# Optimization experiments

Hardware: AMD Instinct MI355X
Metric: run time of the kernel (lower is better)

Reference implementation:

```python
import jax, jax.numpy as jnp
import numpy as np

DIM = 1024
N_HEADS = 16
HEAD_DIM = DIM // N_HEADS
BATCH = 2
SEQ = 2048


def rotate_half(x):
    x1, x2 = jnp.split(x, 2, axis=-1)
    return jnp.concatenate((-x2, x1), axis=-1)


def rope_cos_sin(seq_len, head_dim, dtype=jnp.float32):
    inv_freq = 1.0 / (10000.0 ** (jnp.arange(0, head_dim, 2, dtype=jnp.float32) / head_dim))
    t = jnp.arange(seq_len, dtype=jnp.float32)
    freqs = jnp.einsum('i,j->ij', t, inv_freq)          # [S, hd/2]
    emb = jnp.concatenate((freqs, freqs), axis=-1)       # [S, hd]
    return emb.astype(dtype)[None, :, None, :]           # [1, S, 1, hd] (cos/sin applied below)


def setup_inputs() -> dict:
    key = jax.random.key(0)
    k_x, k_q, k_k, k_v, k_o = jax.random.split(key, 5)
    scale = 1.0 / np.sqrt(DIM)
    x = jax.random.normal(k_x, (BATCH, SEQ, DIM), dtype=jnp.float32)
    Wq = jax.random.normal(k_q, (DIM, DIM), dtype=jnp.float32) * scale
    Wk = jax.random.normal(k_k, (DIM, DIM), dtype=jnp.float32) * scale
    Wv = jax.random.normal(k_v, (DIM, DIM), dtype=jnp.float32) * scale
    Wo = jax.random.normal(k_o, (DIM, DIM), dtype=jnp.float32) * scale
    # causal mask: scores masked where mask == 0
    mask = jnp.tril(jnp.ones((SEQ, SEQ), dtype=jnp.int32))[None, None, :, :]
    return {"x": x, "Wq": Wq, "Wk": Wk, "Wv": Wv, "Wo": Wo, "mask": mask}


def reference(x, Wq, Wk, Wv, Wo, mask):
    B, S, _ = x.shape
    # torch nn.Linear: y = x @ W.T
    q = (x @ Wq.T).reshape(B, S, N_HEADS, HEAD_DIM)
    k = (x @ Wk.T).reshape(B, S, N_HEADS, HEAD_DIM)
    v = (x @ Wv.T).reshape(B, S, N_HEADS, HEAD_DIM)
    ang = rope_cos_sin(S, HEAD_DIM, x.dtype)
    cos, sin = jnp.cos(ang), jnp.sin(ang)
    q = q * cos + rotate_half(q) * sin
    k = k * cos + rotate_half(k) * sin
    # [B, H, S, hd]
    q = q.transpose(0, 2, 1, 3)
    k = k.transpose(0, 2, 1, 3)
    v = v.transpose(0, 2, 1, 3)
    scores = jnp.einsum('bhqd,bhkd->bhqk', q, k) / np.sqrt(HEAD_DIM)
    scores = jnp.where(mask == 0, jnp.asarray(-1e9, scores.dtype), scores)
    attn = jax.nn.softmax(scores, axis=-1)
    out = jnp.einsum('bhqk,bhkd->bhqd', attn, v)
    out = out.transpose(0, 2, 1, 3).reshape(B, S, DIM)
    return out @ Wo.T
```

## Files before the change

### kernel.cpp

```cpp
#include <hip/hip_runtime.h>
#include <stdint.h>

typedef unsigned short u16;
typedef __bf16 bf16x8 __attribute__((ext_vector_type(8)));
typedef __bf16 bf16x4 __attribute__((ext_vector_type(4)));
typedef float f32x4 __attribute__((ext_vector_type(4)));

#define N_B 2
#define N_S 2048
#define N_D 1024
#define N_H 16
#define HD 64

#if __has_builtin(__builtin_amdgcn_exp2f)
#define EXP2F(x) __builtin_amdgcn_exp2f(x)
#else
#define EXP2F(x) exp2f(x)
#endif

__device__ __forceinline__ u16 f2bf(float f) {
  union { float f; uint32_t u; } v; v.f = f;
  uint32_t u = v.u + 0x7fffu + ((v.u >> 16) & 1u);
  return (u16)(u >> 16);
}

__device__ __forceinline__ void gload16(const u16* g, u16* lds) {
  __builtin_amdgcn_global_load_lds(
      (const __attribute__((address_space(1))) unsigned int*)g,
      (__attribute__((address_space(3))) unsigned int*)lds, 16, 0, 0);
}

__global__ __launch_bounds__(256) void prep_kernel(
    const float* __restrict__ x, const float* __restrict__ Wq,
    const float* __restrict__ Wk, const float* __restrict__ Wv,
    const float* __restrict__ Wo,
    u16* __restrict__ xb, u16* __restrict__ wqb, u16* __restrict__ wkb,
    u16* __restrict__ wvb, u16* __restrict__ wob,
    float* __restrict__ cosT, float* __restrict__ sinT)
{
  const int NX = N_B * N_S * N_D;
  const int NW = N_D * N_D;
  int bid = blockIdx.x;
  if (bid < 8192) {
    int i = (bid * 256 + threadIdx.x) * 4;
    const float* src; u16* dst; int off;
    if (i < NX) { src = x; dst = xb; off = i; }
    else {
      int j = i - NX;
      int w = j >> 20;
      off = j & (NW - 1);
      src = (w == 0) ? Wq : (w == 1) ? Wk : (w == 2) ? Wv : Wo;
      dst = (w == 0) ? wqb : (w == 1) ? wkb : (w == 2) ? wvb : wob;
    }
    float4 v = *(const float4*)(src + off);
    ushort4 o;
    o.x = f2bf(v.x); o.y = f2bf(v.y); o.z = f2bf(v.z); o.w = f2bf(v.w);
    *(ushort4*)(dst + off) = o;
  } else {
    int t = (bid - 8192) * 256 + threadIdx.x;
    int s = t >> 5, i = t & 31;
    float inv = expf(-(float)i * 0.28782313662425574f);
    float a = (float)s * inv;
    float sn, cs;
    sincosf(a, &sn, &cs);
    cosT[t] = cs;
    sinT[t] = sn;
  }
}

__global__ __launch_bounds__(256, 5) void proj_kernel(
    const u16* __restrict__ x, const u16* __restrict__ Wq,
    const u16* __restrict__ Wk, const u16* __restrict__ Wv,
    u16* __restrict__ Qb, u16* __restrict__ Kb, u16* __restrict__ Vtb,
    const float* __restrict__ cosT, const float* __restrict__ sinT)
{
  const int mode = blockIdx.z;
  const u16* Wm = (mode == 0) ? Wq : (mode == 1) ? Wk : Wv;
  const int bx = blockIdx.x, by = blockIdx.y;
  const int tid = threadIdx.x;
  const int wave = tid >> 6, lane = tid & 63;
  const int c = lane & 15, quad = lane >> 4;

  __shared__ __align__(16) u16 As[128 * 64];
  __shared__ __align__(16) u16 Bs[64 * 64];

  const f32x4 zero = {0.f, 0.f, 0.f, 0.f};
  f32x4 acc[2][4];
#pragma unroll
  for (int i = 0; i < 2; ++i)
#pragma unroll
    for (int j = 0; j < 4; ++j) acc[i][j] = zero;

  for (int kt = 0; kt < 16; ++kt) {
    const int k0 = kt * 64;
    __syncthreads();
#pragma unroll
    for (int t = 0; t < 4; ++t) {
      int p = t * 256 + tid;
      int m = p >> 3, sl = p & 7;
      int kq = sl ^ (m & 7);
      gload16(x + (size_t)(by * 128 + m) * N_D + k0 + kq * 8, &As[(t * 256 + wave * 64) * 8]);
    }
#pragma unroll
    for (int t = 0; t < 2; ++t) {
      int p = t * 256 + tid;
      int m = p >> 3, sl = p & 7;
      int kq = sl ^ (m & 7);
      gload16(Wm + (size_t)(bx * 64 + m) * N_D + k0 + kq * 8, &Bs[(t * 256 + wave * 64) * 8]);
    }
    __syncthreads();
#pragma unroll
    for (int ks = 0; ks < 2; ++ks) {
      bf16x8 av[2], bv[4];
      int kq = ks * 4 + quad;
#pragma unroll
      for (int i = 0; i < 2; ++i) {
        int m = wave * 32 + i * 16 + c;
        av[i] = *(const bf16x8*)&As[(m * 8 + (kq ^ (m & 7))) * 8];
      }
#pragma unroll
      for (int j = 0; j < 4; ++j) {
        int n = j * 16 + c;
        bv[j] = *(const bf16x8*)&Bs[(n * 8 + (kq ^ (n & 7))) * 8];
      }
#pragma unroll
      for (int i = 0; i < 2; ++i)
#pragma unroll
        for (int j = 0; j < 4; ++j)
          acc[i][j] = __builtin_amdgcn_mfma_f32_16x16x32_bf16(av[i], bv[j], acc[i][j], 0, 0, 0);
    }
  }

  const int h = bx;
  if (mode < 2) {
    u16* Out = (mode == 0) ? Qb : Kb;
#pragma unroll
    for (int i = 0; i < 2; ++i) {
#pragma unroll
      for (int r = 0; r < 4; ++r) {
        int row = by * 128 + wave * 32 + i * 16 + quad * 4 + r;
        int b = row >> 11, s = row & 2047;
        float cs0 = cosT[s * 32 + c],      sn0 = sinT[s * 32 + c];
        float cs1 = cosT[s * 32 + 16 + c], sn1 = sinT[s * 32 + 16 + c];
        size_t base = ((size_t)(b * N_H + h) * N_S + s) * HD;
#pragma unroll
        for (int j = 0; j < 4; ++j) {
          float v = acc[i][j][r];
          float p = acc[i][j ^ 2][r];
          float cs = (j & 1) ? cs1 : cs0;
          float sn = (j & 1) ? sn1 : sn0;
          float res = (j < 2) ? (v * cs - p * sn) : (v * cs + p * sn);
          Out[base + j * 16 + c] = f2bf(res);
        }
      }
    }
  } else {
#pragma unroll
    for (int i = 0; i < 2; ++i) {
      int srow = by * 128 + wave * 32 + i * 16 + quad * 4;
      int b = srow >> 11, sb = srow & 2047;
#pragma unroll
      for (int j = 0; j < 4; ++j) {
        int d = j * 16 + c;
        ushort4 pk;
        pk.x = f2bf(acc[i][j][0]);
        pk.y = f2bf(acc[i][j][1]);
        pk.z = f2bf(acc[i][j][2]);
        pk.w = f2bf(acc[i][j][3]);
        *(ushort4*)&Vtb[((size_t)(b * N_H + h) * HD + d) * N_S + sb] = pk;
      }
    }
  }
}

__global__ __launch_bounds__(64, 3) void attn_kernel(
    const u16* __restrict__ Qb, const u16* __restrict__ Kb,
    const u16* __restrict__ Vtb, u16* __restrict__ Ab)
{
  const int lane = threadIdx.x;
  const int c = lane & 15, quad = lane >> 4;
  const int bx = blockIdx.x;
  const int xcd = bx & 7;
  const int idx = bx >> 3;
  const int t = 63 - (idx >> 2);
  const int bh = xcd + (idx & 3) * 8;
  const int q0 = t * 32;
  const int ktmax = t;

  __shared__ __align__(16) u16 Ks[32 * 64];
  __shared__ __align__(16) u16 Vs[64 * 32];
  __shared__ __align__(16) u16 Ps[32 * 32];

  const u16* Qg = Qb + ((size_t)bh * N_S + q0) * HD;
  const u16* Kg = Kb + (size_t)bh * N_S * HD;
  const u16* Vg = Vtb + (size_t)bh * HD * N_S;

  bf16x8 qreg[2][2];
#pragma unroll
  for (int jQ = 0; jQ < 2; ++jQ)
#pragma unroll
    for (int ks = 0; ks < 2; ++ks)
      qreg[jQ][ks] = *(const bf16x8*)(Qg + (jQ * 16 + c) * HD + ks * 32 + quad * 8);

  const f32x4 zero = {0.f, 0.f, 0.f, 0.f};
  f32x4 acc_o[2][4];
#pragma unroll
  for (int mt = 0; mt < 2; ++mt)
#pragma unroll
    for (int nt = 0; nt < 4; ++nt) acc_o[mt][nt] = zero;
  float lrow[2] = {0.f, 0.f};

  const float CLOG = 0.18033688011112042f;
  const float FM = 16.0f;

  for (int kt = 0; kt <= ktmax; ++kt) {
    asm volatile("s_waitcnt lgkmcnt(0)" ::: "memory");
#pragma unroll
    for (int i = 0; i < 4; ++i) {
      int ci = i * 64 + lane;
      int m = ci >> 3, sl = ci & 7;
      int kq = sl ^ (m & 7);
      gload16(Kg + (size_t)(kt * 32 + m) * HD + kq * 8, &Ks[i * 512]);
    }
#pragma unroll
    for (int i = 0; i < 4; ++i) {
      int ci = i * 64 + lane;
      int d = ci >> 2, sl = ci & 3;
      int kq = sl ^ (d & 3);
      gload16(Vg + (size_t)d * N_S + kt * 32 + kq * 8, &Vs[i * 512]);
    }
    asm volatile("s_waitcnt vmcnt(4)" ::: "memory");

    f32x4 acc_s[2][2];
#pragma unroll
    for (int iK = 0; iK < 2; ++iK)
#pragma unroll
      for (int jQ = 0; jQ < 2; ++jQ) acc_s[iK][jQ] = zero;
#pragma unroll
    for (int ks = 0; ks < 2; ++ks) {
      bf16x8 kf[2];
      int kq = ks * 4 + quad;
#pragma unroll
      for (int iK = 0; iK < 2; ++iK) {
        int m = iK * 16 + c;
        kf[iK] = *(const bf16x8*)&Ks[(m * 8 + (kq ^ (m & 7))) * 8];
      }
#pragma unroll
      for (int iK = 0; iK < 2; ++iK)
#pragma unroll
        for (int jQ = 0; jQ < 2; ++jQ)
          acc_s[iK][jQ] = __builtin_amdgcn_mfma_f32_16x16x32_bf16(
              kf[iK], qreg[jQ][ks], acc_s[iK][jQ], 0, 0, 0);
    }

    const bool domask = (kt == ktmax);
#pragma unroll
    for (int iK = 0; iK < 2; ++iK)
#pragma unroll
      for (int jQ = 0; jQ < 2; ++jQ) {
        bf16x4 pb;
#pragma unroll
        for (int rr = 0; rr < 4; ++rr) {
          float arg = fmaf(acc_s[iK][jQ][rr], CLOG, -FM);
          if (domask) {
            int dsk = iK * 16 + quad * 4 + rr;
            int dq = jQ * 16 + c;
            if (dsk > dq) arg = -3.0e38f;
          }
          float p = EXP2F(arg);
          lrow[jQ] += p;
          pb[rr] = (__bf16)p;
        }
        int q = jQ * 16 + c;
        int slot = (iK * 2 + (quad >> 1)) ^ (q & 3);
        *(bf16x4*)&Ps[q * 32 + slot * 8 + (quad & 1) * 4] = pb;
      }

    asm volatile("s_waitcnt vmcnt(0)" ::: "memory");

    bf16x8 pf[2], vf[4];
#pragma unroll
    for (int nt = 0; nt < 4; ++nt) {
      int d = nt * 16 + c;
      vf[nt] = *(const bf16x8*)&Vs[(d * 4 + (quad ^ (d & 3))) * 8];
    }
#pragma unroll
    for (int mt = 0; mt < 2; ++mt) {
      int q = mt * 16 + c;
      pf[mt] = *(const bf16x8*)&Ps[q * 32 + ((quad ^ (q & 3)) * 8)];
    }
#pragma unroll
    for (int mt = 0; mt < 2; ++mt)
#pragma unroll
      for (int nt = 0; nt < 4; ++nt)
        acc_o[mt][nt] = __builtin_amdgcn_mfma_f32_16x16x32_bf16(
            pf[mt], vf[nt], acc_o[mt][nt], 0, 0, 0);
  }

#pragma unroll
  for (int jQ = 0; jQ < 2; ++jQ) {
    float l = lrow[jQ];
    l += __shfl_xor(l, 16, 64);
    l += __shfl_xor(l, 32, 64);
    lrow[jQ] = 1.0f / l;
  }
  const int b = bh >> 4, h = bh & 15;
#pragma unroll
  for (int mt = 0; mt < 2; ++mt) {
#pragma unroll
    for (int rr = 0; rr < 4; ++rr) {
      float inv = __shfl(lrow[mt], quad * 4 + rr, 64);
      int q = q0 + mt * 16 + quad * 4 + rr;
#pragma unroll
      for (int nt = 0; nt < 4; ++nt) {
        Ab[((size_t)(b * N_S + q)) * N_D + h * HD + nt * 16 + c] =
            f2bf(acc_o[mt][nt][rr] * inv);
      }
    }
  }
}

__global__ __launch_bounds__(256) void out_gemm_kernel(
    const u16* __restrict__ A, const u16* __restrict__ Wo, float* __restrict__ out)
{
  const int bx = blockIdx.x, by = blockIdx.y;
  const int tid = threadIdx.x;
  const int wave = tid >> 6, lane = tid & 63;
  const int c = lane & 15, quad = lane >> 4;
  const int wm = wave & 1, wn = wave >> 1;

  __shared__ __align__(16) u16 As[64 * 64];
  __shared__ __align__(16) u16 Bs[64 * 64];

  const f32x4 zero = {0.f, 0.f, 0.f, 0.f};
  f32x4 acc[2][2];
#pragma unroll
  for (int i = 0; i < 2; ++i)
#pragma unroll
    for (int j = 0; j < 2; ++j) acc[i][j] = zero;

  for (int kt = 0; kt < 16; ++kt) {
    const int k0 = kt * 64;
    __syncthreads();
#pragma unroll
    for (int t = 0; t < 2; ++t) {
      int p = t * 256 + tid;
      int m = p >> 3, sl = p & 7;
      int kq = sl ^ (m & 7);
      gload16(A + (size_t)(by * 64 + m) * N_D + k0 + kq * 8, &As[(t * 256 + wave * 64) * 8]);
    }
#pragma unroll
    for (int t = 0; t < 2; ++t) {
      int p = t * 256 + tid;
      int m = p >> 3, sl = p & 7;
      int kq = sl ^ (m & 7);
      gload16(Wo + (size_t)(bx * 64 + m) * N_D + k0 + kq * 8, &Bs[(t * 256 + wave * 64) * 8]);
    }
    __syncthreads();
#pragma unroll
    for (int ks = 0; ks < 2; ++ks) {
      bf16x8 av[2], bv[2];
      int kq = ks * 4 + quad;
#pragma unroll
      for (int i = 0; i < 2; ++i) {
        int m = wm * 32 + i * 16 + c;
        av[i] = *(const bf16x8*)&As[(m * 8 + (kq ^ (m & 7))) * 8];
      }
#pragma unroll
      for (int j = 0; j < 2; ++j) {
        int n = wn * 32 + j * 16 + c;
        bv[j] = *(const bf16x8*)&Bs[(n * 8 + (kq ^ (n & 7))) * 8];
      }
#pragma unroll
      for (int i = 0; i < 2; ++i)
#pragma unroll
        for (int j = 0; j < 2; ++j)
          acc[i][j] = __builtin_amdgcn_mfma_f32_16x16x32_bf16(av[i], bv[j], acc[i][j], 0, 0, 0);
    }
  }

#pragma unroll
  for (int i = 0; i < 2; ++i)
#pragma unroll
    for (int r = 0; r < 4; ++r) {
      int row = by * 64 + wm * 32 + i * 16 + quad * 4 + r;
#pragma unroll
      for (int j = 0; j < 2; ++j) {
        int col = bx * 64 + wn * 32 + j * 16 + c;
        out[(size_t)row * N_D + col] = acc[i][j][r];
      }
    }
}

extern "C" void kernel_launch(void* const* d_in, const int* in_sizes, int n_in,
                              void* d_out, int out_size, void* d_ws, size_t ws_size,
                              hipStream_t stream) {
  const float* x  = (const float*)d_in[0];
  const float* Wq = (const float*)d_in[1];
  const float* Wk = (const float*)d_in[2];
  const float* Wv = (const float*)d_in[3];
  const float* Wo = (const float*)d_in[4];
  float* out = (float*)d_out;
  char* ws = (char*)d_ws;
  u16* xb   = (u16*)(ws);
  u16* Wqb  = (u16*)(ws + ( 8u << 20));
  u16* Wkb  = (u16*)(ws + (10u << 20));
  u16* Wvb  = (u16*)(ws + (12u << 20));
  u16* Wob  = (u16*)(ws + (14u << 20));
  u16* Qb   = (u16*)(ws + (16u << 20));
  u16* Kb   = (u16*)(ws + (24u << 20));
  u16* Vtb  = (u16*)(ws + (32u << 20));
  u16* Ab   = (u16*)(ws + (40u << 20));
  float* cosT = (float*)(ws + (48u << 20));
  float* sinT = (float*)(ws + (48u << 20) + (1u << 20));

  prep_kernel<<<8448, 256, 0, stream>>>(x, Wq, Wk, Wv, Wo,
                                        xb, Wqb, Wkb, Wvb, Wob, cosT, sinT);
  proj_kernel<<<dim3(16, 32, 3), 256, 0, stream>>>(xb, Wqb, Wkb, Wvb, Qb, Kb, Vtb, cosT, sinT);
  attn_kernel<<<2048, 64, 0, stream>>>(Qb, Kb, Vtb, Ab);
  out_gemm_kernel<<<dim3(16, 64), 256, 0, stream>>>(Ab, Wob, out);
}
```

Before: 207.4 us.

## Double-buffer K tiles in LDS and load V directly into registers

The attention loop now processes 64 keys per iteration as two 32-key chunks. K tiles are double-buffered in shared memory, with the next tile prefetched while the current one is computed. V fragments are read straight from global memory into registers for the next iteration instead of being staged through LDS. The diagonal tile skips its fully masked chunk. The cost is higher register pressure (launch bounds drop from 3 to 2 waves) and the loss of the LDS barrier-style waits around the P buffer, which could risk hazards.

Result: faster. 199.8 us (-3.7%).

```diff
diff --git a/kernel.cpp b/kernel.cpp
--- a/kernel.cpp
+++ b/kernel.cpp
@@ -173,7 +173,7 @@
   }
 }
 
-__global__ __launch_bounds__(64, 3) void attn_kernel(
+__global__ __launch_bounds__(64, 2) void attn_kernel(
     const u16* __restrict__ Qb, const u16* __restrict__ Kb,
     const u16* __restrict__ Vtb, u16* __restrict__ Ab)
 {
@@ -185,10 +185,10 @@
   const int t = 63 - (idx >> 2);
   const int bh = xcd + (idx & 3) * 8;
   const int q0 = t * 32;
-  const int ktmax = t;
-
-  __shared__ __align__(16) u16 Ks[32 * 64];
-  __shared__ __align__(16) u16 Vs[64 * 32];
+  const int ktmax = t >> 1;
+  const int maskch = t & 1;
+
+  __shared__ __align__(16) u16 Ks[2][64 * 64];
   __shared__ __align__(16) u16 Ps[32 * 32];
 
   const u16* Qg = Qb + ((size_t)bh * N_S + q0) * HD;
@@ -213,88 +213,110 @@
   const float CLOG = 0.18033688011112042f;
   const float FM = 16.0f;
 
+#pragma unroll
+  for (int i = 0; i < 8; ++i) {
+    int ci = i * 64 + lane;
+    int m = ci >> 3, sl = ci & 7;
+    int kq = sl ^ (m & 7);
+    gload16(Kg + (size_t)m * HD + kq * 8, &Ks[0][i * 512]);
+  }
+  asm volatile("" ::: "memory");
+  bf16x8 vf[2][4];
+#pragma unroll
+  for (int ch = 0; ch < 2; ++ch)
+#pragma unroll
+    for (int nt = 0; nt < 4; ++nt)
+      vf[ch][nt] = *(const bf16x8*)(Vg + (size_t)(nt * 16 + c) * N_S + ch * 32 + quad * 8);
+
   for (int kt = 0; kt <= ktmax; ++kt) {
-    asm volatile("s_waitcnt lgkmcnt(0)" ::: "memory");
-#pragma unroll
-    for (int i = 0; i < 4; ++i) {
-      int ci = i * 64 + lane;
-      int m = ci >> 3, sl = ci & 7;
-      int kq = sl ^ (m & 7);
-      gload16(Kg + (size_t)(kt * 32 + m) * HD + kq * 8, &Ks[i * 512]);
-    }
-#pragma unroll
-    for (int i = 0; i < 4; ++i) {
-      int ci = i * 64 + lane;
-      int d = ci >> 2, sl = ci & 3;
-      int kq = sl ^ (d & 3);
-      gload16(Vg + (size_t)d * N_S + kt * 32 + kq * 8, &Vs[i * 512]);
-    }
-    asm volatile("s_waitcnt vmcnt(4)" ::: "memory");
-
-    f32x4 acc_s[2][2];
-#pragma unroll
-    for (int iK = 0; iK < 2; ++iK)
-#pragma unroll
-      for (int jQ = 0; jQ < 2; ++jQ) acc_s[iK][jQ] = zero;
-#pragma unroll
-    for (int ks = 0; ks < 2; ++ks) {
-      bf16x8 kf[2];
-      int kq = ks * 4 + quad;
-#pragma unroll
-      for (int iK = 0; iK < 2; ++iK) {
-        int m = iK * 16 + c;
-        kf[iK] = *(const bf16x8*)&Ks[(m * 8 + (kq ^ (m & 7))) * 8];
-      }
-#pragma unroll
-      for (int iK = 0; iK < 2; ++iK)
-#pragma unroll
-        for (int jQ = 0; jQ < 2; ++jQ)
-          acc_s[iK][jQ] = __builtin_amdgcn_mfma_f32_16x16x32_bf16(
-              kf[iK], qreg[jQ][ks], acc_s[iK][jQ], 0, 0, 0);
-    }
-
-    const bool domask = (kt == ktmax);
-#pragma unroll
-    for (int iK = 0; iK < 2; ++iK)
-#pragma unroll
-      for (int jQ = 0; jQ < 2; ++jQ) {
-        bf16x4 pb;
-#pragma unroll
-        for (int rr = 0; rr < 4; ++rr) {
-          float arg = fmaf(acc_s[iK][jQ][rr], CLOG, -FM);
-          if (domask) {
-            int dsk = iK * 16 + quad * 4 + rr;
-            int dq = jQ * 16 + c;
-            if (dsk > dq) arg = -3.0e38f;
+    const u16* kb = &Ks[kt & 1][0];
+    if (kt < ktmax) {
+#pragma unroll
+      for (int i = 0; i < 8; ++i) {
+        int ci = i * 64 + lane;
+        int m = ci >> 3, sl = ci & 7;
+        int kq = sl ^ (m & 7);
+        gload16(Kg + (size_t)((kt + 1) * 64 + m) * HD + kq * 8, &Ks[(kt + 1) & 1][i * 512]);
+      }
+      asm volatile("s_waitcnt vmcnt(16)" ::: "memory");
+    } else {
+      asm volatile("s_waitcnt vmcnt(8)" ::: "memory");
+    }
+
+    const bool diag = (kt == ktmax);
+    const int nch = (diag && maskch == 0) ? 1 : 2;
+
+#pragma unroll
+    for (int ch = 0; ch < 2; ++ch) {
+      if (ch < nch) {
+        f32x4 acc_s[2][2];
+#pragma unroll
+        for (int iK = 0; iK < 2; ++iK)
+#pragma unroll
+          for (int jQ = 0; jQ < 2; ++jQ) acc_s[iK][jQ] = zero;
+#pragma unroll
+        for (int ks = 0; ks < 2; ++ks) {
+          bf16x8 kf[2];
+          int kq = ks * 4 + quad;
+#pragma unroll
+          for (int iK = 0; iK < 2; ++iK) {
+            int m = ch * 32 + iK * 16 + c;
+            kf[iK] = *(const bf16x8*)&kb[(m * 8 + (kq ^ (m & 7))) * 8];
           }
-          float p = EXP2F(arg);
-          lrow[jQ] += p;
-          pb[rr] = (__bf16)p;
+#pragma unroll
+          for (int iK = 0; iK < 2; ++iK)
+#pragma unroll
+            for (int jQ = 0; jQ < 2; ++jQ)
+              acc_s[iK][jQ] = __builtin_amdgcn_mfma_f32_16x16x32_bf16(
+                  kf[iK], qreg[jQ][ks], acc_s[iK][jQ], 0, 0, 0);
         }
-        int q = jQ * 16 + c;
-        int slot = (iK * 2 + (quad >> 1)) ^ (q & 3);
-        *(bf16x4*)&Ps[q * 32 + slot * 8 + (quad & 1) * 4] = pb;
-      }
-
-    asm volatile("s_waitcnt vmcnt(0)" ::: "memory");
-
-    bf16x8 pf[2], vf[4];
-#pragma unroll
-    for (int nt = 0; nt < 4; ++nt) {
-      int d = nt * 16 + c;
-      vf[nt] = *(const bf16x8*)&Vs[(d * 4 + (quad ^ (d & 3))) * 8];
-    }
-#pragma unroll
-    for (int mt = 0; mt < 2; ++mt) {
-      int q = mt * 16 + c;
-      pf[mt] = *(const bf16x8*)&Ps[q * 32 + ((quad ^ (q & 3)) * 8)];
-    }
-#pragma unroll
-    for (int mt = 0; mt < 2; ++mt)
-#pragma unroll
-      for (int nt = 0; nt < 4; ++nt)
-        acc_o[mt][nt] = __builtin_amdgcn_mfma_f32_16x16x32_bf16(
-            pf[mt], vf[nt], acc_o[mt][nt], 0, 0, 0);
+
+        const bool domask = diag && (ch == maskch);
+#pragma unroll
+        for (int iK = 0; iK < 2; ++iK)
+#pragma unroll
+          for (int jQ = 0; jQ < 2; ++jQ) {
+            bf16x4 pb;
+#pragma unroll
+            for (int rr = 0; rr < 4; ++rr) {
+              float arg = fmaf(acc_s[iK][jQ][rr], CLOG, -FM);
+              if (domask) {
+                int dsk = iK * 16 + quad * 4 + rr;
+                int dq = jQ * 16 + c;
+                if (dsk > dq) arg = -3.0e38f;
+              }
+              float p = EXP2F(arg);
+              lrow[jQ] += p;
+              pb[rr] = (__bf16)p;
+            }
+            int q = jQ * 16 + c;
+            int slot = (iK * 2 + (quad >> 1)) ^ (q & 3);
+            *(bf16x4*)&Ps[q * 32 + slot * 8 + (quad & 1) * 4] = pb;
+          }
+
+        bf16x8 pf[2];
+#pragma unroll
+        for (int mt = 0; mt < 2; ++mt) {
+          int q = mt * 16 + c;
+          pf[mt] = *(const bf16x8*)&Ps[q * 32 + ((quad ^ (q & 3)) * 8)];
+        }
+#pragma unroll
+        for (int mt = 0; mt < 2; ++mt)
+#pragma unroll
+          for (int nt = 0; nt < 4; ++nt)
+            acc_o[mt][nt] = __builtin_amdgcn_mfma_f32_16x16x32_bf16(
+                pf[mt], vf[ch][nt], acc_o[mt][nt], 0, 0, 0);
+      }
+    }
+
+    if (kt < ktmax) {
+#pragma unroll
+      for (int ch = 0; ch < 2; ++ch)
+#pragma unroll
+        for (int nt = 0; nt < 4; ++nt)
+          vf[ch][nt] = *(const bf16x8*)(Vg + (size_t)(nt * 16 + c) * N_S
+                                        + (kt + 1) * 64 + ch * 32 + quad * 8);
+    }
   }
 
 #pragma unroll
```
